# Kernel optimization log

Measured on AMD Instinct MI355X. Metric: run time of the kernel, lower is better.

Reference implementation:

```python
import jax, jax.numpy as jnp
import numpy as np

X_SCALE, X_ZP = 0.03, -66.0
Y_SCALE, Y_ZP = 0.025, 160.0  # per-tensor quant params for uint8 y


def setup_inputs() -> dict:
    key = jax.random.key(0)
    kx, ky = jax.random.split(key)
    # x simulates int8 values in [-128, 127], stored as fp32
    x = jax.random.randint(kx, (7, 8, 1024, 1024), 0, 256).astype(jnp.float32) - 128.0
    # y simulates uint8 values in [0, 255], stored as fp32
    y = jax.random.randint(ky, (8, 1024, 1024), 0, 256).astype(jnp.float32)
    return {"x": x, "y": y}


def reference(x, y):
    # dequantize: (q - zero_point) * scale
    qx = (x - X_ZP) * X_SCALE              # [7, B, M, K] fp32
    qy = (y - Y_ZP) * Y_SCALE              # [B, K, N] fp32
    # torch.matmul broadcasting: 4D @ 3D -> [7, B, M, N]
    return jnp.einsum('sbmk,bkn->sbmn', qx, qy)
```

## Files before the change

### kernel.cpp

```cpp
#include <hip/hip_runtime.h>
#include <cstdint>


#define NG 56

typedef int v4i  __attribute__((ext_vector_type(4)));
typedef int v16i __attribute__((ext_vector_type(16)));

#define GLOAD16(g, l) __builtin_amdgcn_global_load_lds( \
    (const __attribute__((address_space(1))) void*)(g), \
    (__attribute__((address_space(3))) void*)(l), 16, 0, 0)

#define MFMA_I8(a, b, c) __builtin_amdgcn_mfma_i32_32x32x32_i8(a, b, c, 0, 0, 0)

typedef __attribute__((address_space(3))) const unsigned char* lds_cptr;

__device__ __forceinline__ v4i lds_read16(lds_cptr p) {
    v4i d;
    asm volatile("ds_read_b128 %0, %1" : "=v"(d) : "v"(p));
    return d;
}

__device__ __forceinline__ unsigned pack4(float4 v, float& s) {
    s += (v.x + v.y) + (v.z + v.w);
    unsigned b0 = __float_as_uint(v.x + 8388736.0f);
    unsigned b1 = __float_as_uint(v.y + 8388736.0f);
    unsigned b2 = __float_as_uint(v.z + 8388736.0f);
    unsigned b3 = __float_as_uint(v.w + 8388736.0f);
    return ((b0 & 0xFFu) | ((b1 & 0xFFu) << 8) | ((b2 & 0xFFu) << 16) | ((b3 & 0xFFu) << 24))
           ^ 0x80808080u;
}

__global__ __launch_bounds__(256) void k_prep_x(const float* __restrict__ x,
                                                unsigned char* __restrict__ xb,
                                                float* __restrict__ rx) {
    int row  = blockIdx.x * 4 + (threadIdx.x >> 6);
    int lane = threadIdx.x & 63;
    const float* src = x + (size_t)row * 1024;
    float s = 0.f;
#pragma unroll
    for (int it = 0; it < 4; ++it) {
        float4 v = *(const float4*)(src + it * 256 + lane * 4);
        unsigned p = pack4(v, s);
        *(unsigned*)&xb[(size_t)row * 1024 + it * 256 + lane * 4] = p;
    }
#pragma unroll
    for (int off = 32; off > 0; off >>= 1) s += __shfl_down(s, off);
    if (lane == 0) rx[row] = s;
}

__global__ __launch_bounds__(256) void k_prep_y(const float* __restrict__ y,
                                                unsigned char* __restrict__ yt,
                                                float* __restrict__ cy) {
    __shared__ float tile[64][65];
    __shared__ float csum[4][64];
    int b  = blockIdx.x >> 8;
    int t  = blockIdx.x & 255;
    int kt = (t >> 4) * 64, nt = (t & 15) * 64;
    int tx = threadIdx.x & 63;
    int ty = threadIdx.x >> 6;
    const float* src = y + ((size_t)b << 20) + (size_t)kt * 1024 + nt;
    float part = 0.f;
#pragma unroll
    for (int r = 0; r < 16; ++r) {
        int kk = r * 4 + ty;
        float v = src[(size_t)kk * 1024 + tx];
        tile[kk][tx] = v;
        part += v;
    }
    csum[ty][tx] = part;
    __syncthreads();
    if (threadIdx.x < 64) {
        float s = csum[0][tx] + csum[1][tx] + csum[2][tx] + csum[3][tx];
        atomicAdd(&cy[b * 1024 + nt + tx], s);
    }
    int ky = threadIdx.x & 15;
    int ny = threadIdx.x >> 4;
#pragma unroll
    for (int r = 0; r < 4; ++r) {
        int nn = r * 16 + ny;
        unsigned b0 = __float_as_uint(tile[ky * 4 + 0][nn] + 8388608.0f);
        unsigned b1 = __float_as_uint(tile[ky * 4 + 1][nn] + 8388608.0f);
        unsigned b2 = __float_as_uint(tile[ky * 4 + 2][nn] + 8388608.0f);
        unsigned b3 = __float_as_uint(tile[ky * 4 + 3][nn] + 8388608.0f);
        unsigned p = ((b0 & 0xFFu) | ((b1 & 0xFFu) << 8) | ((b2 & 0xFFu) << 16) |
                      ((b3 & 0xFFu) << 24)) ^ 0x80808080u;
        *(unsigned*)&yt[((size_t)b << 20) + (size_t)(nt + nn) * 1024 + kt + ky * 4] = p;
    }
}

__global__ __launch_bounds__(256, 3) void k_gemm(const unsigned char* __restrict__ xb,
                                                 const unsigned char* __restrict__ yt,
                                                 const float* __restrict__ rx,
                                                 const float* __restrict__ cy,
                                                 float* __restrict__ out) {
    __shared__ __align__(16) unsigned char As[3][128 * 64];
    __shared__ __align__(16) unsigned char Bs[3][128 * 64];

    int bid = blockIdx.x;
    int wg  = (bid & 7) * (NG * 64 / 8) + (bid >> 3);
    int g   = wg >> 6;
    int t   = wg & 63;
    int m0  = (t >> 3) * 128, n0 = (t & 7) * 128;
    int b   = g & 7;

    int tid = threadIdx.x, lane = tid & 63, w = tid >> 6;
    int wm = w >> 1, wn = w & 1;

    const unsigned char* Ab = xb + (size_t)g * 1048576 + (size_t)m0 * 1024;
    const unsigned char* Bb = yt + ((size_t)b << 20) + (size_t)n0 * 1024;

    int srow   = tid >> 2;
    int schunk = (tid & 3) ^ ((srow >> 1) & 3);
    size_t off0 = (size_t)srow * 1024 + schunk * 16;
    size_t off1 = off0 + 64 * 1024;
    int dst0 = (tid & ~63) * 16;
    int dst1 = (256 + (tid & ~63)) * 16;

#define STAGE(buf, kt) do {                                   \
    GLOAD16(Ab + off0 + (size_t)(kt) * 64, &As[buf][dst0]);   \
    GLOAD16(Ab + off1 + (size_t)(kt) * 64, &As[buf][dst1]);   \
    GLOAD16(Bb + off0 + (size_t)(kt) * 64, &Bs[buf][dst0]);   \
    GLOAD16(Bb + off1 + (size_t)(kt) * 64, &Bs[buf][dst1]);   \
} while (0)

    v16i acc[2][2];
#pragma unroll
    for (int i = 0; i < 2; ++i)
#pragma unroll
        for (int j = 0; j < 2; ++j)
#pragma unroll
            for (int q = 0; q < 16; ++q) acc[i][j][q] = 0;

    int arow = lane & 31, hi = lane >> 5, key = (lane >> 1) & 3;
    int rA0 = (wm * 64 + arow) * 64, rA1 = rA0 + 32 * 64;
    int rB0 = (wn * 64 + arow) * 64, rB1 = rB0 + 32 * 64;
    int c0 = (hi ^ key) * 16;
    int c1 = ((2 + hi) ^ key) * 16;

#define COMPUTE(bi) do {                                                         \
    lds_cptr ap = (lds_cptr)&As[bi][0];                                          \
    lds_cptr bp = (lds_cptr)&Bs[bi][0];                                          \
    v4i a0k0 = lds_read16(ap + rA0 + c0);                                        \
    v4i a1k0 = lds_read16(ap + rA1 + c0);                                        \
    v4i b0k0 = lds_read16(bp + rB0 + c0);                                        \
    v4i b1k0 = lds_read16(bp + rB1 + c0);                                        \
    v4i a0k1 = lds_read16(ap + rA0 + c1);                                        \
    v4i a1k1 = lds_read16(ap + rA1 + c1);                                        \
    v4i b0k1 = lds_read16(bp + rB0 + c1);                                        \
    v4i b1k1 = lds_read16(bp + rB1 + c1);                                        \
    asm volatile("s_waitcnt lgkmcnt(0)" ::: "memory");                           \
    __builtin_amdgcn_sched_barrier(0);                                           \
    acc[0][0] = MFMA_I8(a0k0, b0k0, acc[0][0]);                                  \
    acc[0][1] = MFMA_I8(a0k0, b1k0, acc[0][1]);                                  \
    acc[1][0] = MFMA_I8(a1k0, b0k0, acc[1][0]);                                  \
    acc[1][1] = MFMA_I8(a1k0, b1k0, acc[1][1]);                                  \
    acc[0][0] = MFMA_I8(a0k1, b0k1, acc[0][0]);                                  \
    acc[0][1] = MFMA_I8(a0k1, b1k1, acc[0][1]);                                  \
    acc[1][0] = MFMA_I8(a1k1, b0k1, acc[1][0]);                                  \
    acc[1][1] = MFMA_I8(a1k1, b1k1, acc[1][1]);                                  \
} while (0)

    STAGE(0, 0);
    STAGE(1, 1);

    int cur = 0, nxt = 2;
    for (int kt = 0; kt < 14; ++kt) {
        asm volatile("s_waitcnt vmcnt(4)" ::: "memory");
        __builtin_amdgcn_s_barrier();
        __builtin_amdgcn_sched_barrier(0);
        STAGE(nxt, kt + 2);
        COMPUTE(cur);
        cur = (cur == 2) ? 0 : cur + 1;
        nxt = (nxt == 2) ? 0 : nxt + 1;
    }
    asm volatile("s_waitcnt vmcnt(4)" ::: "memory");
    __builtin_amdgcn_s_barrier();
    __builtin_amdgcn_sched_barrier(0);
    COMPUTE(2);
    asm volatile("s_waitcnt vmcnt(0)" ::: "memory");
    __builtin_amdgcn_s_barrier();
    __builtin_amdgcn_sched_barrier(0);
    COMPUTE(0);
#undef COMPUTE
#undef STAGE

    const float* rxp = rx + g * 1024 + m0 + wm * 64;
    const float* cyp = cy + b * 1024 + n0 + wn * 64;
    float* og = out + (size_t)g * 1048576 + (size_t)(m0 + wm * 64) * 1024 + n0 + wn * 64;
    int col = lane & 31, r4 = hi * 4;
#pragma unroll
    for (int fi = 0; fi < 2; ++fi)
#pragma unroll
        for (int fj = 0; fj < 2; ++fj) {
            int cc = fj * 32 + col;
            float cv = cyp[cc];
            v16i v = acc[fi][fj];
#pragma unroll
            for (int q = 0; q < 16; ++q) {
                int rl = (q & 3) + 8 * (q >> 2) + r4;
                float rxv = rxp[fi * 32 + rl];
                og[(size_t)(fi * 32 + rl) * 1024 + cc] =
                    7.5e-4f * ((float)v[q] - 32.0f * rxv + 66.0f * cv - 10813440.0f);
            }
        }
}

__global__ void k_naive(const float* __restrict__ x, const float* __restrict__ y,
                        float* __restrict__ out) {
    int g = blockIdx.z, b = g & 7;
    int tx = threadIdx.x, ty = threadIdx.y;
    int m = blockIdx.y * 16 + ty, n = blockIdx.x * 16 + tx;
    __shared__ float a[16][17], bs[16][17];
    float s = 0.f;
    for (int kt = 0; kt < 64; ++kt) {
        a[ty][tx]  = x[(size_t)g * 1048576 + (size_t)m * 1024 + kt * 16 + tx];
        bs[ty][tx] = y[(size_t)b * 1048576 + (size_t)(kt * 16 + ty) * 1024 + n];
        __syncthreads();
#pragma unroll
        for (int j = 0; j < 16; ++j)
            s += ((a[ty][j] + 66.0f) * 0.03f) * ((bs[j][tx] - 160.0f) * 0.025f);
        __syncthreads();
    }
    out[(size_t)g * 1048576 + (size_t)m * 1024 + n] = s;
}

extern "C" void kernel_launch(void* const* d_in, const int* in_sizes, int n_in,
                              void* d_out, int out_size, void* d_ws, size_t ws_size,
                              hipStream_t stream) {
    const float* x = (const float*)d_in[0];
    const float* y = (const float*)d_in[1];
    float* out = (float*)d_out;

    const size_t CY_OFF = 0;
    const size_t RX_OFF = 32768;
    const size_t YT_OFF = 262144;
    const size_t XB_OFF = 262144 + 8388608ull;
    const size_t NEED   = XB_OFF + 58720256ull;

    if (ws_size >= NEED) {
        float* cy         = (float*)((char*)d_ws + CY_OFF);
        float* rx         = (float*)((char*)d_ws + RX_OFF);
        unsigned char* yt = (unsigned char*)((char*)d_ws + YT_OFF);
        unsigned char* xb = (unsigned char*)((char*)d_ws + XB_OFF);
        hipMemsetAsync(cy, 0, 32768, stream);
        k_prep_x<<<14336, 256, 0, stream>>>(x, xb, rx);
        k_prep_y<<<2048, 256, 0, stream>>>(y, yt, cy);
        k_gemm<<<NG * 64, 256, 0, stream>>>(xb, yt, rx, cy, out);
    } else {
        dim3 grid(64, 64, NG), blk(16, 16);
        k_naive<<<grid, blk, 0, stream>>>(x, y, out);
    }
}
```

Measured before the change: 195.3 us.

## Enlarge GEMM tile to 256x256 with 512 threads and phased LDS prefetch pipeline

The int8 GEMM workgroup tile grows from 128x128 to 256x256, using 8 waves (2x4), each computing 128x64. The main loop is split into four phases per k-tile. Each phase prefetches LDS fragments into registers while running MFMAs on the previous fragments, interleaves the global-to-LDS loads, and raises wave priority around MFMA bursts. The aim is more operand reuse per byte loaded and overlap of LDS reads with MFMA. The cost is a larger LDS footprint (96KB), more barriers per k-tile, and lower occupancy.

```diff
diff --git a/kernel.cpp b/kernel.cpp
--- a/kernel.cpp
+++ b/kernel.cpp
@@ -89,108 +89,141 @@
     }
 }
 
-__global__ __launch_bounds__(256, 3) void k_gemm(const unsigned char* __restrict__ xb,
+__global__ __launch_bounds__(512, 2) void k_gemm(const unsigned char* __restrict__ xb,
                                                  const unsigned char* __restrict__ yt,
                                                  const float* __restrict__ rx,
                                                  const float* __restrict__ cy,
                                                  float* __restrict__ out) {
-    __shared__ __align__(16) unsigned char As[3][128 * 64];
-    __shared__ __align__(16) unsigned char Bs[3][128 * 64];
+    __shared__ __align__(16) unsigned char As[3][256 * 64];
+    __shared__ __align__(16) unsigned char Bs[3][256 * 64];
 
     int bid = blockIdx.x;
-    int wg  = (bid & 7) * (NG * 64 / 8) + (bid >> 3);
-    int g   = wg >> 6;
-    int t   = wg & 63;
-    int m0  = (t >> 3) * 128, n0 = (t & 7) * 128;
+    int wg  = (bid & 7) * 112 + (bid >> 3);
+    int g   = wg >> 4;
+    int t   = wg & 15;
+    int m0  = (t >> 2) * 256, n0 = (t & 3) * 256;
     int b   = g & 7;
 
     int tid = threadIdx.x, lane = tid & 63, w = tid >> 6;
-    int wm = w >> 1, wn = w & 1;
+    int wm = w >> 2, wn = w & 3;
 
     const unsigned char* Ab = xb + (size_t)g * 1048576 + (size_t)m0 * 1024;
     const unsigned char* Bb = yt + ((size_t)b << 20) + (size_t)n0 * 1024;
 
     int srow   = tid >> 2;
     int schunk = (tid & 3) ^ ((srow >> 1) & 3);
-    size_t off0 = (size_t)srow * 1024 + schunk * 16;
-    size_t off1 = off0 + 64 * 1024;
-    int dst0 = (tid & ~63) * 16;
-    int dst1 = (256 + (tid & ~63)) * 16;
-
-#define STAGE(buf, kt) do {                                   \
-    GLOAD16(Ab + off0 + (size_t)(kt) * 64, &As[buf][dst0]);   \
-    GLOAD16(Ab + off1 + (size_t)(kt) * 64, &As[buf][dst1]);   \
-    GLOAD16(Bb + off0 + (size_t)(kt) * 64, &Bs[buf][dst0]);   \
-    GLOAD16(Bb + off1 + (size_t)(kt) * 64, &Bs[buf][dst1]);   \
-} while (0)
-
-    v16i acc[2][2];
-#pragma unroll
-    for (int i = 0; i < 2; ++i)
+    size_t offA0 = (size_t)srow * 1024 + (size_t)schunk * 16;
+    size_t offA1 = offA0 + 131072;
+    int dstA0 = (tid & ~63) * 16;
+    int dstA1 = 8192 + (tid & ~63) * 16;
+
+#define GLQ0(rs, kb) GLOAD16(Ab + offA0 + (size_t)(kb), &As[rs][dstA0])
+#define GLQ1(rs, kb) GLOAD16(Ab + offA1 + (size_t)(kb), &As[rs][dstA1])
+#define GLQ2(rs, kb) GLOAD16(Bb + offA0 + (size_t)(kb), &Bs[rs][dstA0])
+#define GLQ3(rs, kb) GLOAD16(Bb + offA1 + (size_t)(kb), &Bs[rs][dstA1])
+
+    v16i acc[4][2];
+#pragma unroll
+    for (int i = 0; i < 4; ++i)
 #pragma unroll
         for (int j = 0; j < 2; ++j)
 #pragma unroll
             for (int q = 0; q < 16; ++q) acc[i][j][q] = 0;
 
     int arow = lane & 31, hi = lane >> 5, key = (lane >> 1) & 3;
-    int rA0 = (wm * 64 + arow) * 64, rA1 = rA0 + 32 * 64;
-    int rB0 = (wn * 64 + arow) * 64, rB1 = rB0 + 32 * 64;
+    int rA0 = (wm * 128 +  0 + arow) * 64;
+    int rA1 = (wm * 128 + 32 + arow) * 64;
+    int rA2 = (wm * 128 + 64 + arow) * 64;
+    int rA3 = (wm * 128 + 96 + arow) * 64;
+    int rB0 = (wn * 64 +  0 + arow) * 64;
+    int rB1 = (wn * 64 + 32 + arow) * 64;
     int c0 = (hi ^ key) * 16;
     int c1 = ((2 + hi) ^ key) * 16;
 
-#define COMPUTE(bi) do {                                                         \
-    lds_cptr ap = (lds_cptr)&As[bi][0];                                          \
-    lds_cptr bp = (lds_cptr)&Bs[bi][0];                                          \
-    v4i a0k0 = lds_read16(ap + rA0 + c0);                                        \
-    v4i a1k0 = lds_read16(ap + rA1 + c0);                                        \
-    v4i b0k0 = lds_read16(bp + rB0 + c0);                                        \
-    v4i b1k0 = lds_read16(bp + rB1 + c0);                                        \
-    v4i a0k1 = lds_read16(ap + rA0 + c1);                                        \
-    v4i a1k1 = lds_read16(ap + rA1 + c1);                                        \
-    v4i b0k1 = lds_read16(bp + rB0 + c1);                                        \
-    v4i b1k1 = lds_read16(bp + rB1 + c1);                                        \
-    asm volatile("s_waitcnt lgkmcnt(0)" ::: "memory");                           \
-    __builtin_amdgcn_sched_barrier(0);                                           \
-    acc[0][0] = MFMA_I8(a0k0, b0k0, acc[0][0]);                                  \
-    acc[0][1] = MFMA_I8(a0k0, b1k0, acc[0][1]);                                  \
-    acc[1][0] = MFMA_I8(a1k0, b0k0, acc[1][0]);                                  \
-    acc[1][1] = MFMA_I8(a1k0, b1k0, acc[1][1]);                                  \
-    acc[0][0] = MFMA_I8(a0k1, b0k1, acc[0][0]);                                  \
-    acc[0][1] = MFMA_I8(a0k1, b1k1, acc[0][1]);                                  \
-    acc[1][0] = MFMA_I8(a1k1, b0k1, acc[1][0]);                                  \
-    acc[1][1] = MFMA_I8(a1k1, b1k1, acc[1][1]);                                  \
+    v4i cA0, cA1, cB0, cB1;
+    v4i nA0, nA1, nB0, nB1;
+
+#define VM3 asm volatile("s_waitcnt vmcnt(3)" ::: "memory")
+#define VM0 asm volatile("s_waitcnt vmcnt(0)" ::: "memory")
+#define NOVM (void)0
+
+#define PHASE(VMS, RN, CK, RAa, RAb, N0, N1, N2, N3, GLS, LGK, HH, C0_, C1_, C2_, C3_) do { \
+    VMS;                                                                   \
+    __builtin_amdgcn_s_barrier();                                          \
+    __builtin_amdgcn_sched_barrier(0);                                     \
+    { lds_cptr _ap = (lds_cptr)&As[RN][0];                                 \
+      lds_cptr _bp = (lds_cptr)&Bs[RN][0];                                 \
+      N0 = lds_read16(_ap + RAa + (CK));                                   \
+      N1 = lds_read16(_ap + RAb + (CK));                                   \
+      N2 = lds_read16(_bp + rB0 + (CK));                                   \
+      N3 = lds_read16(_bp + rB1 + (CK)); }                                 \
+    GLS;                                                                   \
+    asm volatile("s_waitcnt lgkmcnt(" #LGK ")" ::: "memory");              \
+    __builtin_amdgcn_sched_barrier(0);                                     \
+    __builtin_amdgcn_s_setprio(1);                                         \
+    acc[2*(HH)  ][0] = MFMA_I8(C0_, C2_, acc[2*(HH)  ][0]);                \
+    acc[2*(HH)  ][1] = MFMA_I8(C0_, C3_, acc[2*(HH)  ][1]);                \
+    acc[2*(HH)+1][0] = MFMA_I8(C1_, C2_, acc[2*(HH)+1][0]);                \
+    acc[2*(HH)+1][1] = MFMA_I8(C1_, C3_, acc[2*(HH)+1][1]);                \
+    __builtin_amdgcn_s_setprio(0);                                         \
 } while (0)
 
-    STAGE(0, 0);
-    STAGE(1, 1);
-
-    int cur = 0, nxt = 2;
-    for (int kt = 0; kt < 14; ++kt) {
-        asm volatile("s_waitcnt vmcnt(4)" ::: "memory");
-        __builtin_amdgcn_s_barrier();
-        __builtin_amdgcn_sched_barrier(0);
-        STAGE(nxt, kt + 2);
-        COMPUTE(cur);
-        cur = (cur == 2) ? 0 : cur + 1;
-        nxt = (nxt == 2) ? 0 : nxt + 1;
-    }
+#define TILE(rt, rn, rs, DOST, VMP3) do {                                                       \
+    PHASE(NOVM, rt, c0, rA2, rA3, nA0,nA1,nB0,nB1, if (DOST) GLQ0(rs, kb);, 4, 0, cA0,cA1,cB0,cB1); \
+    PHASE(NOVM, rt, c1, rA0, rA1, cA0,cA1,cB0,cB1, if (DOST) GLQ1(rs, kb);, 4, 1, nA0,nA1,nB0,nB1); \
+    PHASE(NOVM, rt, c1, rA2, rA3, nA0,nA1,nB0,nB1, if (DOST) GLQ2(rs, kb);, 4, 0, cA0,cA1,cB0,cB1); \
+    PHASE(VMP3, rn, c0, rA0, rA1, cA0,cA1,cB0,cB1, if (DOST) GLQ3(rs, kb);, 4, 1, nA0,nA1,nB0,nB1); \
+} while (0)
+
+    GLQ0(0, 0);  GLQ1(0, 0);  GLQ2(0, 0);  GLQ3(0, 0);
+    GLQ0(1, 64); GLQ1(1, 64); GLQ2(1, 64); GLQ3(1, 64);
+    VM3; VM0;
     asm volatile("s_waitcnt vmcnt(4)" ::: "memory");
     __builtin_amdgcn_s_barrier();
     __builtin_amdgcn_sched_barrier(0);
-    COMPUTE(2);
-    asm volatile("s_waitcnt vmcnt(0)" ::: "memory");
+    { lds_cptr _ap = (lds_cptr)&As[0][0];
+      lds_cptr _bp = (lds_cptr)&Bs[0][0];
+      cA0 = lds_read16(_ap + rA0 + c0);
+      cA1 = lds_read16(_ap + rA1 + c0);
+      cB0 = lds_read16(_bp + rB0 + c0);
+      cB1 = lds_read16(_bp + rB1 + c0); }
+
+    int kb = 128;
+    for (int u = 0; u < 4; ++u) {
+        TILE(0, 1, 2, 1, VM3); kb += 64;
+        TILE(1, 2, 0, 1, VM3); kb += 64;
+        TILE(2, 0, 1, 1, VM3); kb += 64;
+    }
+    TILE(0, 1, 2, 1, VM3); kb += 64;
+    TILE(1, 2, 0, 1, VM3); kb += 64;
+    TILE(2, 0, 1, 0, VM0);
+    PHASE(NOVM, 0, c0, rA2, rA3, nA0,nA1,nB0,nB1, NOVM;, 4, 0, cA0,cA1,cB0,cB1);
+    PHASE(NOVM, 0, c1, rA0, rA1, cA0,cA1,cB0,cB1, NOVM;, 4, 1, nA0,nA1,nB0,nB1);
+    PHASE(NOVM, 0, c1, rA2, rA3, nA0,nA1,nB0,nB1, NOVM;, 4, 0, cA0,cA1,cB0,cB1);
     __builtin_amdgcn_s_barrier();
     __builtin_amdgcn_sched_barrier(0);
-    COMPUTE(0);
-#undef COMPUTE
-#undef STAGE
-
-    const float* rxp = rx + g * 1024 + m0 + wm * 64;
+    asm volatile("s_waitcnt lgkmcnt(0)" ::: "memory");
+    __builtin_amdgcn_sched_barrier(0);
+    acc[2][0] = MFMA_I8(nA0, nB0, acc[2][0]);
+    acc[2][1] = MFMA_I8(nA0, nB1, acc[2][1]);
+    acc[3][0] = MFMA_I8(nA1, nB0, acc[3][0]);
+    acc[3][1] = MFMA_I8(nA1, nB1, acc[3][1]);
+#undef TILE
+#undef PHASE
+#undef VM3
+#undef VM0
+#undef NOVM
+#undef GLQ0
+#undef GLQ1
+#undef GLQ2
+#undef GLQ3
+
+    const float* rxp = rx + g * 1024 + m0 + wm * 128;
     const float* cyp = cy + b * 1024 + n0 + wn * 64;
-    float* og = out + (size_t)g * 1048576 + (size_t)(m0 + wm * 64) * 1024 + n0 + wn * 64;
+    float* og = out + (size_t)g * 1048576 + (size_t)(m0 + wm * 128) * 1024 + n0 + wn * 64;
     int col = lane & 31, r4 = hi * 4;
 #pragma unroll
-    for (int fi = 0; fi < 2; ++fi)
+    for (int fi = 0; fi < 4; ++fi)
 #pragma unroll
         for (int fj = 0; fj < 2; ++fj) {
             int cc = fj * 32 + col;
@@ -246,7 +279,7 @@
         hipMemsetAsync(cy, 0, 32768, stream);
         k_prep_x<<<14336, 256, 0, stream>>>(x, xb, rx);
         k_prep_y<<<2048, 256, 0, stream>>>(y, yt, cy);
-        k_gemm<<<NG * 64, 256, 0, stream>>>(xb, yt, rx, cy, out);
+        k_gemm<<<NG * 16, 512, 0, stream>>>(xb, yt, rx, cy, out);
     } else {
         dim3 grid(64, 64, NG), blk(16, 16);
         k_naive<<<grid, blk, 0, stream>>>(x, y, out);
```

After: 181.9 us, median of 5. 6.8% less time.
